# Performance work log

Hardware: AMD Instinct MI355X
Metric: run time of the kernel (lower is better)

Reference implementation:

```python
import jax, jax.numpy as jnp
import numpy as np

B, LS, LW, D = 4, 160, 128, 768
POS_DIM = WD = PWD = DDD = 64
MAX_SPAN = 8
NZ = int(LW * 0.5)          # span_pruned_threshold = 0.5
HID = 128
SPAN_DIM = 2 * D + 2 * POS_DIM + WD      # 1728
PAIR_DIM = 2 * SPAN_DIM + PWD + DDD      # 3584
BINS = np.array([0, 1, 2, 3, 4, 5, 6, 7, 8, 9, 10, 15, 20, 25, 30, 50, 80])

def _span_indices(n, max_span):
    # enumeration order matches the torch loop: window = 1..max_span, start ascending
    s, e = [], []
    for w in range(1, min(n, max_span) + 1):
        st = np.arange(n - w + 1)
        s.append(st); e.append(st + w - 1)
    return np.concatenate(s), np.concatenate(e)

STARTS, ENDS = _span_indices(LW, MAX_SPAN)   # [S], S = 996
NUM_SPANS = len(STARTS)
WIDTH_IDS = np.searchsorted(BINS, ENDS - STARTS + 1, side='right') - 1  # bucket_embedding


def setup_inputs() -> dict:
    key = jax.random.key(0)
    ks = jax.random.split(key, 20)
    w = lambda k, shape, s=0.05: (jax.random.normal(k, shape, dtype=jnp.float32) * s)
    return {
        "last_hidden": jax.random.normal(ks[0], (B, LS, D), dtype=jnp.float32),
        "bert_subword_mask_matrix": jax.random.uniform(ks[1], (B, LS, LS), dtype=jnp.float32),
        "word_len": jnp.ones((B, LW), dtype=jnp.float32),
        "pos_table": w(ks[2], (50, POS_DIM), 1.0),
        "width_table": w(ks[3], (17, WD), 1.0),
        "rel_table": w(ks[4], (17, PWD), 1.0),
        "dep_table": w(ks[5], (30, DDD), 1.0),
        "sW1": w(ks[6], (SPAN_DIM, HID)), "sb1": jnp.zeros((HID,), jnp.float32),
        "sW2": w(ks[7], (HID, HID)),      "sb2": jnp.zeros((HID,), jnp.float32),
        "sW3": w(ks[8], (HID, 3)),        "sb3": jnp.zeros((3,), jnp.float32),
        "pW1": w(ks[9], (PAIR_DIM, HID)), "pb1": jnp.zeros((HID,), jnp.float32),
        "pW2": w(ks[10], (HID, HID)),     "pb2": jnp.zeros((HID,), jnp.float32),
        "pW3": w(ks[11], (HID, 4)),       "pb3": jnp.zeros((4,), jnp.float32),
        "first_subword_seq": jnp.sort(jax.random.randint(ks[12], (B, LW), 0, LS), axis=-1),
        "pos_id": jax.random.randint(ks[13], (B, LW), 0, 50),
        "dep_dis": jax.random.randint(ks[14], (B, LW, LW), 0, 30),
    }


def _ffnn(x, W1, b1, W2, b2, W3, b3):
    h = jax.nn.relu(x @ W1 + b1)
    h = jax.nn.relu(h @ W2 + b2)
    return h @ W3 + b3          # dropout is identity in eval mode


def reference(last_hidden, bert_subword_mask_matrix, word_len,
              pos_table, width_table, rel_table, dep_table,
              sW1, sb1, sW2, sb2, sW3, sb3,
              pW1, pb1, pW2, pb2, pW3, pb3,
              first_subword_seq, pos_id, dep_dis):
    # subword -> word features
    feats = jnp.einsum('bst,btd->bsd', bert_subword_mask_matrix, last_hidden)   # [B,LS,D]
    feats = jnp.take_along_axis(feats, first_subword_seq[:, :, None], axis=1)   # [B,LW,D]
    feats = feats / word_len[:, :, None]
    pos_feats = pos_table[pos_id]                                               # [B,LW,64]

    # span representation: [x_i; x_j; p_i; p_j; width_emb]
    w_emb = width_table[WIDTH_IDS]                                              # [S,64]
    spans = jnp.concatenate([
        feats[:, STARTS], feats[:, ENDS],
        pos_feats[:, STARTS], pos_feats[:, ENDS],
        jnp.broadcast_to(w_emb[None], (B, NUM_SPANS, WD))], axis=-1)            # [B,S,1728]

    span_prob = _ffnn(spans, sW1, sb1, sW2, sb2, sW3, sb3)                       # [B,S,3]

    # pruned target/opinion spans
    t_idx = jax.lax.top_k(span_prob[:, :, 1], NZ)[1]                             # [B,NZ]
    o_idx = jax.lax.top_k(span_prob[:, :, 2], NZ)[1]
    t_pair = jnp.repeat(t_idx, NZ, axis=1)                                       # itertools.product order
    o_pair = jnp.tile(o_idx, (1, NZ))                                            # [B,P], P = NZ*NZ

    starts = jnp.asarray(STARTS); ends = jnp.asarray(ENDS)
    a, b = starts[t_pair], ends[t_pair]
    c, d = starts[o_pair], ends[o_pair]

    # f_distance: min(|b-c|, |a-d|), bucketed
    rel = jnp.minimum(jnp.abs(b - c), jnp.abs(a - d))
    rel_ids = jnp.searchsorted(jnp.asarray(BINS), rel, side='right') - 1
    rel_emb = rel_table[rel_ids]                                                 # [B,P,64]

    # dep distance: min of dep_dis[a:b+1, c:d+1]
    BIG = jnp.int32(2 ** 30)
    dep_pad = jnp.pad(dep_dis.astype(jnp.int32),
                      ((0, 0), (0, MAX_SPAN), (0, MAX_SPAN)), constant_values=2 ** 30)
    r = jnp.arange(MAX_SPAN)

    def block_min(dm, ai, bi, ci, di):
        blk = jax.lax.dynamic_slice(dm, (ai, ci), (MAX_SPAN, MAX_SPAN))
        mask = (r[:, None] <= bi - ai) & (r[None, :] <= di - ci)
        return jnp.min(jnp.where(mask, blk, BIG))

    dep_ids = jax.vmap(jax.vmap(block_min, in_axes=(None, 0, 0, 0, 0)),
                       in_axes=(0, 0, 0, 0, 0))(dep_pad, a, b, c, d)             # [B,P]
    dep_emb = dep_table[dep_ids]                                                 # [B,P,64]

    span_t = jnp.take_along_axis(spans, t_pair[:, :, None], axis=1)              # [B,P,1728]
    span_o = jnp.take_along_axis(spans, o_pair[:, :, None], axis=1)
    pair_feat = jnp.concatenate([span_t, span_o, rel_emb, dep_emb], axis=-1)     # [B,P,3584]

    pair_prob = _ffnn(pair_feat, pW1, pb1, pW2, pb2, pW3, pb3)                   # [B,P,4]
    return span_prob, pair_prob
```

## Files before the change

kernel.cpp:

```cpp
#include <hip/hip_runtime.h>

#define BB 4
#define LS 160
#define LW 128
#define DD 768
#define NSPANS 996
#define NZv 64
#define NPAIR 4096
#define HID 128
#define XLD 832
#define PROJ_N 393216


__device__ inline void span_decode(int s, int& st, int& en, int& w) {
  int ww = 1, base = 0;
  while (ww < 8 && s >= base + (129 - ww)) { base += 129 - ww; ++ww; }
  st = s - base; en = st + ww - 1; w = ww;
}

__device__ inline int bucket17(int v) {
  const int BINSv[17] = {0,1,2,3,4,5,6,7,8,9,10,15,20,25,30,50,80};
  int r = 0;
#pragma unroll
  for (int k = 1; k < 17; ++k) r += (v >= BINSv[k]) ? 1 : 0;
  return r;
}

__global__ __launch_bounds__(256) void prep_kernel(
    const float* __restrict__ mask, const float* __restrict__ lh,
    const int* __restrict__ fss, const float* __restrict__ wlen,
    const int* __restrict__ pos_id, const float* __restrict__ pos_table,
    const float* __restrict__ width_table, const float* __restrict__ rel_table,
    const float* __restrict__ dep_table, const float* __restrict__ sW1,
    const float* __restrict__ pW1, const float* __restrict__ sb1,
    const float* __restrict__ pb1, float* __restrict__ X,
    float* __restrict__ tabs) {
  int gid = blockIdx.x;
  int tid = threadIdx.x;
  if (gid < 96) {
    int nt = gid % 12, mt = gid / 12;
    int b = mt >> 1;
    int row0 = mt * 64, c0 = nt * 64;
    __shared__ float as[16][68];
    __shared__ float bs[16][68];
    __shared__ int fssl[64];
    __shared__ float wll[64];
    if (tid < 64) { fssl[tid] = fss[row0 + tid]; wll[tid] = wlen[row0 + tid]; }
    __syncthreads();
    int rg = tid >> 4, tc = tid & 15;
    float acc[4][4] = {{0.f}};
    for (int k0 = 0; k0 < LS; k0 += 16) {
      {
        int r = tid >> 2, kb = (tid & 3) * 4;
        float4 mv = *(const float4*)(mask + (size_t)(b * LS + fssl[r]) * LS + k0 + kb);
        as[kb + 0][r] = mv.x; as[kb + 1][r] = mv.y;
        as[kb + 2][r] = mv.z; as[kb + 3][r] = mv.w;
      }
      {
        int c = tid & 63, kq = tid >> 6;
#pragma unroll
        for (int q = 0; q < 4; ++q) {
          int kk = kq * 4 + q;
          bs[kk][c] = lh[(size_t)(b * LS + k0 + kk) * DD + c0 + c];
        }
      }
      __syncthreads();
#pragma unroll
      for (int kk = 0; kk < 16; ++kk) {
        float av[4], bv[4];
#pragma unroll
        for (int i = 0; i < 4; ++i) av[i] = as[kk][rg * 4 + i];
#pragma unroll
        for (int j = 0; j < 4; ++j) bv[j] = bs[kk][tc * 4 + j];
#pragma unroll
        for (int i = 0; i < 4; ++i)
#pragma unroll
          for (int j = 0; j < 4; ++j) acc[i][j] += av[i] * bv[j];
      }
      __syncthreads();
    }
#pragma unroll
    for (int i = 0; i < 4; ++i) {
      int r = rg * 4 + i;
      float wl = wll[r];
      float4 v = make_float4(acc[i][0] / wl, acc[i][1] / wl, acc[i][2] / wl, acc[i][3] / wl);
      *(float4*)(X + (size_t)(row0 + r) * XLD + c0 + tc * 4) = v;
    }
  } else if (gid < 104) {
    int e0 = (gid - 96) * 4096 + tid * 16;
    int row = e0 >> 6, c0 = e0 & 63;
    const float* src = pos_table + pos_id[row] * 64 + c0;
    float* dst = X + (size_t)row * XLD + 768 + c0;
#pragma unroll
    for (int q = 0; q < 4; ++q)
      *(float4*)(dst + q * 4) = *(const float4*)(src + q * 4);
  } else {
    int bt = gid - 104;
    const float *src, *W, *bias; int rows; float* o;
    switch (bt) {
      case 0: src = width_table; W = sW1 + 1664 * HID; bias = sb1;    rows = 17; o = tabs;        break;
      case 1: src = width_table; W = pW1 + 1664 * HID; bias = nullptr; rows = 17; o = tabs + 2176; break;
      case 2: src = width_table; W = pW1 + 3392 * HID; bias = nullptr; rows = 17; o = tabs + 4352; break;
      case 3: src = rel_table;   W = pW1 + 3456 * HID; bias = nullptr; rows = 17; o = tabs + 6528; break;
      default:src = dep_table;   W = pW1 + 3520 * HID; bias = pb1;    rows = 30; o = tabs + 8704; break;
    }
    for (int e = tid; e < rows * HID; e += 256) {
      int r = e >> 7, c = e & 127;
      float acc = 0.f;
#pragma unroll 8
      for (int k = 0; k < 64; ++k) acc += src[r * 64 + k] * W[k * HID + c];
      o[e] = acc + (bias ? bias[c] : 0.f);
    }
  }
}

__global__ __launch_bounds__(256) void proj_gemm(
    const float* __restrict__ X, const float* __restrict__ sW1,
    const float* __restrict__ pW1, float* __restrict__ part) {
  int nt = blockIdx.x, mt = blockIdx.y, ks = blockIdx.z;
  const int f_offs[6] = {0, 768, 0, 768, 1728, 2496};
  const int p_offs[6] = {1536, 1600, 1536, 1600, 3264, 3328};
  int g = nt >> 1;
  const float* Wb = (g < 2) ? sW1 : pW1;
  int f_off = f_offs[g], p_off = p_offs[g];
  int c0 = (nt & 1) * 64;
  int row0 = mt * 64;
  int kbase = ks * 416;
  __shared__ float as[16][68];
  __shared__ float bs[16][68];
  int tid = threadIdx.x;
  int rg = tid >> 4, tc = tid & 15;
  float acc[4][4] = {{0.f}};
  for (int k0 = 0; k0 < 416; k0 += 16) {
    {
      int r = tid >> 2, kb = (tid & 3) * 4;
      float4 xv = *(const float4*)(X + (size_t)(row0 + r) * XLD + kbase + k0 + kb);
      as[kb + 0][r] = xv.x; as[kb + 1][r] = xv.y;
      as[kb + 2][r] = xv.z; as[kb + 3][r] = xv.w;
    }
    {
      int c = tid & 63, kq = tid >> 6;
#pragma unroll
      for (int q = 0; q < 4; ++q) {
        int kk = kq * 4 + q;
        int kg = kbase + k0 + kk;
        int wr = (kg < 768) ? (f_off + kg) : (p_off + kg - 768);
        bs[kk][c] = Wb[(size_t)wr * HID + c0 + c];
      }
    }
    __syncthreads();
#pragma unroll
    for (int kk = 0; kk < 16; ++kk) {
      float av[4], bv[4];
#pragma unroll
      for (int i = 0; i < 4; ++i) av[i] = as[kk][rg * 4 + i];
#pragma unroll
      for (int j = 0; j < 4; ++j) bv[j] = bs[kk][tc * 4 + j];
#pragma unroll
      for (int i = 0; i < 4; ++i)
#pragma unroll
        for (int j = 0; j < 4; ++j) acc[i][j] += av[i] * bv[j];
    }
    __syncthreads();
  }
#pragma unroll
  for (int i = 0; i < 4; ++i) {
    int row = row0 + rg * 4 + i;
    int bb = row >> 7, iloc = row & 127;
    float* dst = part + (size_t)ks * PROJ_N +
                 ((size_t)(g * BB + bb) * LW + iloc) * HID + c0 + tc * 4;
    *(float4*)dst = make_float4(acc[i][0], acc[i][1], acc[i][2], acc[i][3]);
  }
}

__global__ __launch_bounds__(256) void span_kernel(
    const float* __restrict__ part, const float* __restrict__ tabs,
    const float* __restrict__ sW2, const float* __restrict__ sb2,
    const float* __restrict__ sW3, const float* __restrict__ sb3,
    float* __restrict__ out) {
  int b = blockIdx.y, s0 = blockIdx.x * 32;
  int cnt = min(32, NSPANS - s0);
  __shared__ float hT[128][36];
  __shared__ float wsh[16][132];
  __shared__ float w3s[384];
  __shared__ int stl[32], enl[32], wdl[32];
  int tid = threadIdx.x;
  if (tid < 32 && tid < cnt) {
    int st, en, w; span_decode(s0 + tid, st, en, w);
    stl[tid] = st; enl[tid] = en; wdl[tid] = w;
  }
  for (int i = tid; i < 384; i += 256) w3s[i] = sW3[i];
  __syncthreads();
  const float* SA0 = part + (size_t)(0 * BB + b) * LW * HID;
  const float* SB0 = part + (size_t)(1 * BB + b) * LW * HID;
  const float* SA1 = SA0 + PROJ_N;
  const float* SB1 = SB0 + PROJ_N;
  const float* SW = tabs;
#pragma unroll
  for (int u = 0; u < 16; ++u) {
    int e = tid + u * 256; int r = e >> 7, c = e & 127;
    float v = 0.f;
    if (r < cnt) {
      int sa = stl[r] * HID + c, sb = enl[r] * HID + c;
      v = ((SA0[sa] + SA1[sa]) + (SB0[sb] + SB1[sb])) + SW[wdl[r] * HID + c];
    }
    hT[c][r] = fmaxf(v, 0.f);
  }
  __syncthreads();
  int rg = tid >> 5, tc = tid & 31;
  float acc[4][4] = {{0.f}};
  for (int k0 = 0; k0 < HID; k0 += 16) {
#pragma unroll
    for (int u = 0; u < 8; ++u) {
      int idx = tid + u * 256; int r = idx >> 7, c = idx & 127;
      wsh[r][c] = sW2[(k0 + r) * HID + c];
    }
    __syncthreads();
#pragma unroll
    for (int kk = 0; kk < 16; ++kk) {
      float4 a4 = *(const float4*)&hT[k0 + kk][rg * 4];
      float4 b4 = *(const float4*)&wsh[kk][tc * 4];
      float av[4] = {a4.x, a4.y, a4.z, a4.w};
      float bv[4] = {b4.x, b4.y, b4.z, b4.w};
#pragma unroll
      for (int i = 0; i < 4; ++i)
#pragma unroll
        for (int j = 0; j < 4; ++j) acc[i][j] += av[i] * bv[j];
    }
    __syncthreads();
  }
#pragma unroll
  for (int i = 0; i < 4; ++i)
#pragma unroll
    for (int j = 0; j < 4; ++j)
      hT[tc * 4 + j][rg * 4 + i] = fmaxf(acc[i][j] + sb2[tc * 4 + j], 0.f);
  __syncthreads();
  if (tid < 96) {
    int sl = tid / 3, oc = tid - sl * 3;
    if (sl < cnt) {
      float a = sb3[oc];
#pragma unroll 16
      for (int k = 0; k < HID; ++k) a += hT[k][sl] * w3s[k * 3 + oc];
      out[(b * NSPANS + s0 + sl) * 3 + oc] = a;
    }
  }
}

struct PairShared {
  union {
    struct { unsigned long long k1[1024]; unsigned long long k2[1024]; } s;
    float hT[128][68];
  } u;
  float wsh[16][132];
  float w3[512];
  int mTA[64], mTB[64], mOA[64], mOB[64], mTW[64], mOW[64], mR[64], mD[64];
  int tixl[64], oixl[64];
};

__global__ __launch_bounds__(256) void pair_kernel(
    const float* __restrict__ part, const float* __restrict__ tabs,
    const int* __restrict__ dep_dis, const float* __restrict__ pW2,
    const float* __restrict__ pb2, const float* __restrict__ pW3,
    const float* __restrict__ pb3, float* __restrict__ out) {
  int b = blockIdx.y, p0 = blockIdx.x * 64;
  __shared__ __align__(16) PairShared sm;
  int tid = threadIdx.x;

  {
    unsigned long long* k1 = sm.u.s.k1;
    unsigned long long* k2 = sm.u.s.k2;
#pragma unroll
    for (int uu = 0; uu < 4; ++uu) {
      int e = tid + uu * 256;
      unsigned long long kk1 = 0ull, kk2 = 0ull;
      if (e < NSPANS) {
        unsigned int b1 = __float_as_uint(out[(b * NSPANS + e) * 3 + 1]);
        unsigned int m1 = (b1 & 0x80000000u) ? ~b1 : (b1 | 0x80000000u);
        kk1 = ((unsigned long long)m1 << 32) | (unsigned long long)(0xFFFFFFFFu - e);
        unsigned int b2 = __float_as_uint(out[(b * NSPANS + e) * 3 + 2]);
        unsigned int m2 = (b2 & 0x80000000u) ? ~b2 : (b2 | 0x80000000u);
        kk2 = ((unsigned long long)m2 << 32) | (unsigned long long)(0xFFFFFFFFu - e);
      }
      k1[e] = kk1; k2[e] = kk2;
    }
    __syncthreads();
    for (int k = 2; k <= 1024; k <<= 1) {
      for (int j = k >> 1; j > 0; j >>= 1) {
#pragma unroll
        for (int uu = 0; uu < 4; ++uu) {
          int i = tid + uu * 256;
          int l = i ^ j;
          if (l > i) {
            bool desc = ((i & k) == 0);
            unsigned long long a1 = k1[i], c1 = k1[l];
            if (desc ? (a1 < c1) : (a1 > c1)) { k1[i] = c1; k1[l] = a1; }
            unsigned long long a2 = k2[i], c2 = k2[l];
            if (desc ? (a2 < c2) : (a2 > c2)) { k2[i] = c2; k2[l] = a2; }
          }
        }
        __syncthreads();
      }
    }
    if (tid < NZv) {
      sm.tixl[tid] = (int)(0xFFFFFFFFu - (unsigned int)k1[tid]);
      sm.oixl[tid] = (int)(0xFFFFFFFFu - (unsigned int)k2[tid]);
    }
    __syncthreads();
  }

  {
    sm.w3[tid] = pW3[tid]; sm.w3[tid + 256] = pW3[tid + 256];
    int m = tid >> 2, sub = tid & 3;
    int p = p0 + m;
    int ti = sm.tixl[p >> 6];
    int oi = sm.oixl[p & 63];
    int a, bb2, wt, c, d, wo;
    span_decode(ti, a, bb2, wt);
    span_decode(oi, c, d, wo);
    int mn = 0x7FFFFFFF;
    const int* dp = dep_dis + b * LW * LW;
    for (int x = a; x <= bb2; ++x)
      for (int y = c + sub; y <= d; y += 4)
        mn = min(mn, dp[x * LW + y]);
    mn = min(mn, __shfl_xor(mn, 1));
    mn = min(mn, __shfl_xor(mn, 2));
    if (sub == 0) {
      int rel = min(abs(bb2 - c), abs(a - d));
      sm.mTA[m] = ((2 * BB + b) * LW + a)   * HID;
      sm.mTB[m] = ((3 * BB + b) * LW + bb2) * HID;
      sm.mOA[m] = ((4 * BB + b) * LW + c)   * HID;
      sm.mOB[m] = ((5 * BB + b) * LW + d)   * HID;
      sm.mTW[m] = 2176 + wt * HID;
      sm.mOW[m] = 4352 + wo * HID;
      sm.mR[m]  = 6528 + bucket17(rel) * HID;
      sm.mD[m]  = 8704 + mn * HID;
    }
  }
  __syncthreads();

#pragma unroll
  for (int uu = 0; uu < 32; ++uu) {
    int e = tid + uu * 256; int r = e >> 7, c = e & 127;
    int ta = sm.mTA[r] + c, tb = sm.mTB[r] + c, oa = sm.mOA[r] + c, ob = sm.mOB[r] + c;
    float v = (part[ta] + part[ta + PROJ_N]) + (part[tb] + part[tb + PROJ_N]) +
              (part[oa] + part[oa + PROJ_N]) + (part[ob] + part[ob + PROJ_N]) +
              tabs[sm.mTW[r] + c] + tabs[sm.mOW[r] + c] +
              tabs[sm.mR[r] + c] + tabs[sm.mD[r] + c];
    sm.u.hT[c][r] = fmaxf(v, 0.f);
  }
  __syncthreads();

  int rg = tid >> 5, tc = tid & 31;
  float acc[8][4] = {{0.f}};
  for (int k0 = 0; k0 < HID; k0 += 16) {
#pragma unroll
    for (int uu = 0; uu < 8; ++uu) {
      int idx = tid + uu * 256; int r = idx >> 7, c = idx & 127;
      sm.wsh[r][c] = pW2[(k0 + r) * HID + c];
    }
    __syncthreads();
#pragma unroll
    for (int kk = 0; kk < 16; ++kk) {
      float4 a0 = *(const float4*)&sm.u.hT[k0 + kk][rg * 8];
      float4 a1 = *(const float4*)&sm.u.hT[k0 + kk][rg * 8 + 4];
      float4 b4 = *(const float4*)&sm.wsh[kk][tc * 4];
      float av[8] = {a0.x, a0.y, a0.z, a0.w, a1.x, a1.y, a1.z, a1.w};
      float bv[4] = {b4.x, b4.y, b4.z, b4.w};
#pragma unroll
      for (int i = 0; i < 8; ++i)
#pragma unroll
        for (int j = 0; j < 4; ++j) acc[i][j] += av[i] * bv[j];
    }
    __syncthreads();
  }
#pragma unroll
  for (int i = 0; i < 8; ++i)
#pragma unroll
    for (int j = 0; j < 4; ++j)
      sm.u.hT[tc * 4 + j][rg * 8 + i] = fmaxf(acc[i][j] + pb2[tc * 4 + j], 0.f);
  __syncthreads();

  {
    int sl = tid >> 2, oc = tid & 3;
    float a = pb3[oc];
#pragma unroll 16
    for (int k = 0; k < HID; ++k) a += sm.u.hT[k][sl] * sm.w3[k * 4 + oc];
    out[BB * NSPANS * 3 + (b * NPAIR + p0 + sl) * 4 + oc] = a;
  }
}

extern "C" void kernel_launch(void* const* d_in, const int* in_sizes, int n_in,
                              void* d_out, int out_size, void* d_ws, size_t ws_size,
                              hipStream_t stream) {
  const float* last_hidden = (const float*)d_in[0];
  const float* mask        = (const float*)d_in[1];
  const float* word_len    = (const float*)d_in[2];
  const float* pos_table   = (const float*)d_in[3];
  const float* width_table = (const float*)d_in[4];
  const float* rel_table   = (const float*)d_in[5];
  const float* dep_table   = (const float*)d_in[6];
  const float* sW1 = (const float*)d_in[7];
  const float* sb1 = (const float*)d_in[8];
  const float* sW2 = (const float*)d_in[9];
  const float* sb2 = (const float*)d_in[10];
  const float* sW3 = (const float*)d_in[11];
  const float* sb3 = (const float*)d_in[12];
  const float* pW1 = (const float*)d_in[13];
  const float* pb1 = (const float*)d_in[14];
  const float* pW2 = (const float*)d_in[15];
  const float* pb2 = (const float*)d_in[16];
  const float* pW3 = (const float*)d_in[17];
  const float* pb3 = (const float*)d_in[18];
  const int* fss     = (const int*)d_in[19];
  const int* pos_id  = (const int*)d_in[20];
  const int* dep_dis = (const int*)d_in[21];

  float* ws   = (float*)d_ws;
  float* X    = ws;
  float* part = ws + 425984;
  float* tabs = ws + 1212416;
  float* out  = (float*)d_out;

  prep_kernel<<<109, 256, 0, stream>>>(mask, last_hidden, fss, word_len,
                                       pos_id, pos_table, width_table, rel_table,
                                       dep_table, sW1, pW1, sb1, pb1, X, tabs);
  proj_gemm<<<dim3(12, 8, 2), 256, 0, stream>>>(X, sW1, pW1, part);
  span_kernel<<<dim3(32, BB), 256, 0, stream>>>(part, tabs, sW2, sb2, sW3, sb3, out);
  pair_kernel<<<dim3(64, BB), 256, 0, stream>>>(part, tabs, dep_dis,
                                                pW2, pb2, pW3, pb3, out);
}
```

Measured before the change: 235.6 us.

## Replace bitonic top-k sort with rank counting in pair kernel

Swaps the shared-memory bitonic sort of both span-score key arrays for a rank computation. Each thread counts how many keys are larger than its own four keys and writes the index directly if the rank is below the top-k cutoff. This removes the roughly fifty-five barrier-separated sort stages in exchange for about a thousand broadcast shared-memory reads per thread. The keys are unique because they embed the span index, so ranks are distinct and the tie order stays the same.

New measurement: 239.9 us. About the same (+1.8%).

```diff
diff --git a/kernel.cpp b/kernel.cpp
--- a/kernel.cpp
+++ b/kernel.cpp
@@ -248,7 +248,7 @@
 
 struct PairShared {
   union {
-    struct { unsigned long long k1[1024]; unsigned long long k2[1024]; } s;
+    unsigned long long keys[2048];
     float hT[128][68];
   } u;
   float wsh[16][132];
@@ -267,43 +267,42 @@
   int tid = threadIdx.x;
 
   {
-    unsigned long long* k1 = sm.u.s.k1;
-    unsigned long long* k2 = sm.u.s.k2;
+    ulonglong2* kp = (ulonglong2*)sm.u.keys;
+    unsigned long long m1[4], m2[4];
 #pragma unroll
     for (int uu = 0; uu < 4; ++uu) {
       int e = tid + uu * 256;
       unsigned long long kk1 = 0ull, kk2 = 0ull;
       if (e < NSPANS) {
         unsigned int b1 = __float_as_uint(out[(b * NSPANS + e) * 3 + 1]);
-        unsigned int m1 = (b1 & 0x80000000u) ? ~b1 : (b1 | 0x80000000u);
-        kk1 = ((unsigned long long)m1 << 32) | (unsigned long long)(0xFFFFFFFFu - e);
+        unsigned int v1 = (b1 & 0x80000000u) ? ~b1 : (b1 | 0x80000000u);
+        kk1 = ((unsigned long long)v1 << 32) | (unsigned long long)(0xFFFFFFFFu - e);
         unsigned int b2 = __float_as_uint(out[(b * NSPANS + e) * 3 + 2]);
-        unsigned int m2 = (b2 & 0x80000000u) ? ~b2 : (b2 | 0x80000000u);
-        kk2 = ((unsigned long long)m2 << 32) | (unsigned long long)(0xFFFFFFFFu - e);
-      }
-      k1[e] = kk1; k2[e] = kk2;
-    }
-    __syncthreads();
-    for (int k = 2; k <= 1024; k <<= 1) {
-      for (int j = k >> 1; j > 0; j >>= 1) {
-#pragma unroll
-        for (int uu = 0; uu < 4; ++uu) {
-          int i = tid + uu * 256;
-          int l = i ^ j;
-          if (l > i) {
-            bool desc = ((i & k) == 0);
-            unsigned long long a1 = k1[i], c1 = k1[l];
-            if (desc ? (a1 < c1) : (a1 > c1)) { k1[i] = c1; k1[l] = a1; }
-            unsigned long long a2 = k2[i], c2 = k2[l];
-            if (desc ? (a2 < c2) : (a2 > c2)) { k2[i] = c2; k2[l] = a2; }
-          }
-        }
-        __syncthreads();
-      }
-    }
-    if (tid < NZv) {
-      sm.tixl[tid] = (int)(0xFFFFFFFFu - (unsigned int)k1[tid]);
-      sm.oixl[tid] = (int)(0xFFFFFFFFu - (unsigned int)k2[tid]);
+        unsigned int v2 = (b2 & 0x80000000u) ? ~b2 : (b2 | 0x80000000u);
+        kk2 = ((unsigned long long)v2 << 32) | (unsigned long long)(0xFFFFFFFFu - e);
+        ulonglong2 kk; kk.x = kk1; kk.y = kk2;
+        kp[e] = kk;
+      }
+      m1[uu] = kk1; m2[uu] = kk2;
+    }
+    __syncthreads();
+    int r1[4] = {0, 0, 0, 0}, r2[4] = {0, 0, 0, 0};
+#pragma unroll 4
+    for (int j = 0; j < NSPANS; ++j) {
+      ulonglong2 a = kp[j];
+#pragma unroll
+      for (int uu = 0; uu < 4; ++uu) {
+        r1[uu] += (a.x > m1[uu]) ? 1 : 0;
+        r2[uu] += (a.y > m2[uu]) ? 1 : 0;
+      }
+    }
+#pragma unroll
+    for (int uu = 0; uu < 4; ++uu) {
+      int e = tid + uu * 256;
+      if (e < NSPANS) {
+        if (r1[uu] < NZv) sm.tixl[r1[uu]] = e;
+        if (r2[uu] < NZv) sm.oixl[r2[uu]] = e;
+      }
     }
     __syncthreads();
   }
```
